# Performance work log

Hardware: AMD Instinct MI355X
Metric: run time of the kernel (lower is better)

## Reference

```python
import jax, jax.numpy as jnp
import numpy as np

DIM = 2048
N_HEADS = 16
HEAD_DIM = DIM // N_HEADS

def setup_inputs() -> dict:
    key = jax.random.key(0)
    kx, kqkv, kout = jax.random.split(key, 3)
    x = jax.random.normal(kx, (2, 2048, DIM), dtype=jnp.float32)
    # nn.Linear weights stored [out_features, in_features]; y = x @ W.T
    W_qkv = jax.random.normal(kqkv, (3 * DIM, DIM), dtype=jnp.float32) * (DIM ** -0.5)
    W_out = jax.random.normal(kout, (DIM, DIM), dtype=jnp.float32) * (DIM ** -0.5)
    return {"x": x, "W_qkv": W_qkv, "W_out": W_out}

def reference(x, W_qkv, W_out):
    B, T, D = x.shape
    qkv = jnp.einsum('btd,ed->bte', x, W_qkv)  # [B,T,3D]
    q, k, v = jnp.split(qkv, 3, axis=-1)
    def heads(t):
        return t.reshape(B, T, N_HEADS, HEAD_DIM).transpose(0, 2, 1, 3)  # [B,H,T,d]
    q, k, v = heads(q), heads(k), heads(v)
    att = jnp.einsum('bhid,bhjd->bhij', q, k) / (HEAD_DIM ** 0.5)
    causal = jnp.tril(jnp.ones((T, T), dtype=bool))
    att = jnp.where(causal, att, -jnp.inf)
    att = jax.nn.softmax(att, axis=-1)
    out = jnp.einsum('bhij,bhjd->bhid', att, v)
    out = out.transpose(0, 2, 1, 3).reshape(B, T, D)
    return jnp.einsum('btd,ed->bte', out, W_out)
```

## Files before the change

kernel.cpp:

```cpp
#include <hip/hip_runtime.h>

typedef short short8 __attribute__((ext_vector_type(8)));
typedef short short4v __attribute__((ext_vector_type(4)));
typedef float f32x4 __attribute__((ext_vector_type(4)));
typedef unsigned short u16;
typedef u16 ushort4v __attribute__((ext_vector_type(4)));

__device__ inline u16 f2bf(float f){
  unsigned int u = __builtin_bit_cast(unsigned int, f);
  u = (u + 0x7fffu + ((u >> 16) & 1u)) >> 16;
  return (u16)u;
}

__device__ inline short8 cat8(short4v a, short4v b){
  short8 r;
  r[0]=a[0]; r[1]=a[1]; r[2]=a[2]; r[3]=a[3];
  r[4]=b[0]; r[5]=b[1]; r[6]=b[2]; r[7]=b[3];
  return r;
}

__device__ inline void gload_lds16(const void* g, unsigned lds_addr){
  __builtin_amdgcn_global_load_lds((__attribute__((address_space(1))) void*)(uintptr_t)g,
                                   (__attribute__((address_space(3))) void*)(uintptr_t)lds_addr,
                                   16, 0, 0);
}

__global__ void cvt_bf16(const float* __restrict__ in, u16* __restrict__ out, int n4){
  int stride = gridDim.x * blockDim.x;
  for (int i = blockIdx.x * blockDim.x + threadIdx.x; i < n4; i += stride){
    float4 v = ((const float4*)in)[i];
    ushort4v r = { f2bf(v.x), f2bf(v.y), f2bf(v.z), f2bf(v.w) };
    ((ushort4v*)out)[i] = r;
  }
}

template<int OUT_BF16>
__global__ __launch_bounds__(512, 2) void gemm_bt2(const u16* __restrict__ A, const u16* __restrict__ B,
                                                   void* __restrict__ Cv, int M, int N, int K){
  __shared__ u16 lds[2][24576];
  const int tid = threadIdx.x, wave = tid >> 6, lane = tid & 63;
  const int lr = lane & 15, lg = lane >> 4;
  const int wm = wave >> 2, wn = wave & 3;
  const long bm = blockIdx.x * 128L, bn = blockIdx.y * 256L;
  const int l3 = lane >> 3, l7 = lane & 7;

  const u16* asrc = A + (bm + wave * 8 + l3) * (long)K + (l7 ^ l3) * 8;
  const u16* bsrc = B + (bn + wave * 8 + l3) * (long)K + (l7 ^ l3) * 8;
  const unsigned ldsbase = (unsigned)(uintptr_t)&lds[0][0];
  const unsigned adst = wave * 1024u;
  const unsigned bdst = 16384u + wave * 1024u;

  #define STAGE(BUF, K0) { \
    unsigned bb = ldsbase + (unsigned)(BUF) * 49152u; \
    gload_lds16(asrc + (K0),                       bb + adst); \
    gload_lds16(asrc + 64 * (size_t)K + (K0),      bb + adst + 8192u); \
    gload_lds16(bsrc + (K0),                       bb + bdst); \
    gload_lds16(bsrc + 64 * (size_t)K + (K0),      bb + bdst + 8192u); \
    gload_lds16(bsrc + 128 * (size_t)K + (K0),     bb + bdst + 16384u); \
    gload_lds16(bsrc + 192 * (size_t)K + (K0),     bb + bdst + 24576u); \
  }

  f32x4 acc[4][4] = {};
  const int nk = K >> 6;
  int cur = 0;

  STAGE(0, 0)
  asm volatile("s_waitcnt vmcnt(0)" ::: "memory");
  __builtin_amdgcn_sched_barrier(0);
  __builtin_amdgcn_s_barrier();
  __builtin_amdgcn_sched_barrier(0);

  for (int t = 0; t < nk; ++t){
    if (t + 1 < nk){
      STAGE(cur ^ 1, (t + 1) * 64)
      asm volatile("s_waitcnt vmcnt(6)" ::: "memory");
    } else {
      asm volatile("s_waitcnt vmcnt(0)" ::: "memory");
    }
    __builtin_amdgcn_sched_barrier(0);
    __builtin_amdgcn_s_barrier();
    __builtin_amdgcn_sched_barrier(0);

    const u16* Ab = &lds[cur][0];
    const u16* Bb = &lds[cur][8192];
    short8 af[2][4], bfr[2][4];
    #pragma unroll
    for (int kk = 0; kk < 2; kk++){
      #pragma unroll
      for (int m = 0; m < 4; m++){
        int row = wm * 64 + m * 16 + lr;
        int phys = (kk * 4 + lg) ^ (row & 7);
        af[kk][m] = *(const short8*)&Ab[row * 64 + phys * 8];
      }
      #pragma unroll
      for (int n = 0; n < 4; n++){
        int row = wn * 64 + n * 16 + lr;
        int phys = (kk * 4 + lg) ^ (row & 7);
        bfr[kk][n] = *(const short8*)&Bb[row * 64 + phys * 8];
      }
    }
    __builtin_amdgcn_s_setprio(1);
    #pragma unroll
    for (int m = 0; m < 4; m++)
      #pragma unroll
      for (int n = 0; n < 4; n++){
        acc[m][n] = __builtin_amdgcn_mfma_f32_16x16x32_bf16(af[0][m], bfr[0][n], acc[m][n], 0, 0, 0);
        acc[m][n] = __builtin_amdgcn_mfma_f32_16x16x32_bf16(af[1][m], bfr[1][n], acc[m][n], 0, 0, 0);
      }
    __builtin_amdgcn_s_setprio(0);

    __builtin_amdgcn_sched_barrier(0);
    __builtin_amdgcn_s_barrier();
    __builtin_amdgcn_sched_barrier(0);
    cur ^= 1;
  }
  #undef STAGE

  #pragma unroll
  for (int m = 0; m < 4; m++){
    #pragma unroll
    for (int n = 0; n < 4; n++){
      #pragma unroll
      for (int r = 0; r < 4; r++){
        long row = bm + wm*64 + m*16 + lg*4 + r;
        long col = bn + wn*64 + n*16 + lr;
        float v = acc[m][n][r];
        if (OUT_BF16) ((u16*)Cv)[row * (long)N + col] = f2bf(v);
        else          ((float*)Cv)[row * (long)N + col] = v;
      }
    }
  }
}

__global__ __launch_bounds__(512, 2) void attn_fwd(const u16* __restrict__ qkv, u16* __restrict__ out){
  const int T = 2048, D3 = 6144, D = 2048, HD = 128;
  const int bh = blockIdx.x;
  const int pr = blockIdx.y;
  const int b = bh >> 4, h = bh & 15;
  const int tid = threadIdx.x, wave = tid >> 6, lane = tid & 63;
  const int lr = lane & 15, lg = lane >> 4;

  __shared__ u16 Klds[64][136];
  __shared__ u16 Vlds[64][136];
  __shared__ u16 Plds[8][16][72];

  const size_t base = (size_t)b * T * D3;
  const unsigned vtr = (unsigned)(uintptr_t)&Vlds[(lane >> 4) * 8 + ((lane >> 2) & 3)][(lane & 3) * 4];

  const int srow = tid >> 4;
  const int scol = (tid & 15) * 8;
  const u16* kgp = qkv + base + (size_t)srow * D3 + D + h * HD + scol;
  const u16* vgp = kgp + D;

  for (int half = 0; half < 2; half++){
    const int qt = half ? pr : (15 - pr);
    const int q0 = qt * 128;
    const int q0w = q0 + wave * 16;

    short8 qf[4];
    {
      const u16* qrow = qkv + base + (size_t)(q0w + lr) * D3 + h * HD;
      #pragma unroll
      for (int kk = 0; kk < 4; kk++)
        qf[kk] = *(const short8*)(qrow + kk*32 + lg*8);
    }

    f32x4 o[8] = {};
    float mrow[4], lrw[4];
    #pragma unroll
    for (int r = 0; r < 4; r++){ mrow[r] = -1e30f; lrw[r] = 0.f; }

    const int ntiles = (q0 + 128) >> 6;
    short8 kreg[2], vreg[2];
    #pragma unroll
    for (int c = 0; c < 2; c++){
      kreg[c] = *(const short8*)(kgp + (size_t)(32 * c) * D3);
      vreg[c] = *(const short8*)(vgp + (size_t)(32 * c) * D3);
    }

    for (int t = 0; t < ntiles; t++){
      const int k0 = t * 64;
      __syncthreads();
      #pragma unroll
      for (int c = 0; c < 2; c++){
        *(short8*)&Klds[srow + 32*c][scol] = kreg[c];
        *(short8*)&Vlds[srow + 32*c][scol] = vreg[c];
      }
      __syncthreads();
      if (t + 1 < ntiles){
        const u16* kn = kgp + (size_t)(k0 + 64) * D3;
        const u16* vn = vgp + (size_t)(k0 + 64) * D3;
        #pragma unroll
        for (int c = 0; c < 2; c++){
          kreg[c] = *(const short8*)(kn + (size_t)(32 * c) * D3);
          vreg[c] = *(const short8*)(vn + (size_t)(32 * c) * D3);
        }
      }

      if (k0 <= q0w + 15){
        f32x4 s[4] = {};
        #pragma unroll
        for (int kh = 0; kh < 4; kh++){
          #pragma unroll
          for (int kk = 0; kk < 4; kk++){
            short8 kfrag = *(const short8*)&Klds[kh*16 + lr][kk*32 + lg*8];
            s[kh] = __builtin_amdgcn_mfma_f32_16x16x32_bf16(qf[kk], kfrag, s[kh], 0, 0, 0);
          }
        }
        const float scale = 0.08838834764831845f;
        const bool need_mask = (k0 + 63 > q0w);
        #pragma unroll
        for (int kh = 0; kh < 4; kh++){
          int key = k0 + kh*16 + lr;
          #pragma unroll
          for (int r = 0; r < 4; r++){
            float v = s[kh][r] * scale;
            if (need_mask && key > q0w + lg*4 + r) v = -1e30f;
            s[kh][r] = v;
          }
        }
        float fs[4];
        #pragma unroll
        for (int r = 0; r < 4; r++){
          float mx = fmaxf(fmaxf(s[0][r], s[1][r]), fmaxf(s[2][r], s[3][r]));
          #pragma unroll
          for (int msk = 8; msk >= 1; msk >>= 1)
            mx = fmaxf(mx, __shfl_xor(mx, msk, 64));
          float mnew = fmaxf(mrow[r], mx);
          float f = __expf(mrow[r] - mnew);
          float p0 = __expf(s[0][r] - mnew);
          float p1 = __expf(s[1][r] - mnew);
          float p2 = __expf(s[2][r] - mnew);
          float p3 = __expf(s[3][r] - mnew);
          s[0][r] = p0; s[1][r] = p1; s[2][r] = p2; s[3][r] = p3;
          float rs = (p0 + p1) + (p2 + p3);
          #pragma unroll
          for (int msk = 8; msk >= 1; msk >>= 1)
            rs += __shfl_xor(rs, msk, 64);
          lrw[r] = lrw[r] * f + rs;
          mrow[r] = mnew;
          fs[r] = f;
        }
        #pragma unroll
        for (int dt = 0; dt < 8; dt++)
          #pragma unroll
          for (int r = 0; r < 4; r++)
            o[dt][r] *= fs[r];
        #pragma unroll
        for (int kh = 0; kh < 4; kh++)
          #pragma unroll
          for (int r = 0; r < 4; r++)
            Plds[wave][lg*4 + r][kh*16 + lr] = f2bf(s[kh][r]);
        asm volatile("s_waitcnt lgkmcnt(0)" ::: "memory");
        __builtin_amdgcn_sched_barrier(0);
        short8 pf[2];
        #pragma unroll
        for (int kp2 = 0; kp2 < 2; kp2++)
          pf[kp2] = *(const short8*)&Plds[wave][lr][kp2*32 + lg*8];
        asm volatile("s_waitcnt lgkmcnt(0)" ::: "memory");
        __builtin_amdgcn_sched_barrier(0);

        short4v vf[2][2][2];
        #define TR4(BUF, PTR) \
          asm volatile("ds_read_b64_tr_b16 %0, %1"             : "=v"(vf[BUF][0][0]) : "v"(PTR)); \
          asm volatile("ds_read_b64_tr_b16 %0, %1 offset:1088" : "=v"(vf[BUF][0][1]) : "v"(PTR)); \
          asm volatile("ds_read_b64_tr_b16 %0, %1 offset:8704" : "=v"(vf[BUF][1][0]) : "v"(PTR)); \
          asm volatile("ds_read_b64_tr_b16 %0, %1 offset:9792" : "=v"(vf[BUF][1][1]) : "v"(PTR));
        TR4(0, vtr)
        #pragma unroll
        for (int dt = 0; dt < 8; dt++){
          if (dt < 7){
            unsigned pn = vtr + (unsigned)((dt + 1) * 32);
            TR4((dt + 1) & 1, pn)
            asm volatile("s_waitcnt lgkmcnt(4)" ::: "memory");
          } else {
            asm volatile("s_waitcnt lgkmcnt(0)" ::: "memory");
          }
          __builtin_amdgcn_sched_barrier(0);
          short8 v0 = cat8(vf[dt & 1][0][0], vf[dt & 1][0][1]);
          short8 v1 = cat8(vf[dt & 1][1][0], vf[dt & 1][1][1]);
          o[dt] = __builtin_amdgcn_mfma_f32_16x16x32_bf16(pf[0], v0, o[dt], 0, 0, 0);
          o[dt] = __builtin_amdgcn_mfma_f32_16x16x32_bf16(pf[1], v1, o[dt], 0, 0, 0);
        }
        #undef TR4
      }
    }
    float rl[4];
    #pragma unroll
    for (int r = 0; r < 4; r++) rl[r] = 1.0f / lrw[r];
    #pragma unroll
    for (int dt = 0; dt < 8; dt++){
      #pragma unroll
      for (int r = 0; r < 4; r++){
        float v = o[dt][r] * rl[r];
        int qa = q0w + lg*4 + r;
        out[(size_t)(b * T + qa) * D + h * HD + dt*16 + lr] = f2bf(v);
      }
    }
  }
}

extern "C" void kernel_launch(void* const* d_in, const int* in_sizes, int n_in,
                              void* d_out, int out_size, void* d_ws, size_t ws_size,
                              hipStream_t stream) {
  const float* x    = (const float*)d_in[0];
  const float* wqkv = (const float*)d_in[1];
  const float* wout = (const float*)d_in[2];
  float* out = (float*)d_out;

  u16* ws    = (u16*)d_ws;
  u16* xb    = ws;
  u16* wqkvb = xb + 8388608;
  u16* qkvb  = wqkvb + 12582912;
  u16* attnb = xb;
  u16* woutb = wqkvb;

  cvt_bf16<<<2048, 256, 0, stream>>>(x,    xb,    8388608 / 4);
  cvt_bf16<<<2048, 256, 0, stream>>>(wqkv, wqkvb, 12582912 / 4);

  gemm_bt2<1><<<dim3(32, 24), 512, 0, stream>>>(xb, wqkvb, qkvb, 4096, 6144, 2048);

  cvt_bf16<<<2048, 256, 0, stream>>>(wout, woutb, 4194304 / 4);

  attn_fwd<<<dim3(32, 8), 512, 0, stream>>>(qkvb, attnb);

  gemm_bt2<0><<<dim3(32, 8), 512, 0, stream>>>(attnb, woutb, out, 4096, 2048, 2048);
}
```

Measured before the change: 268.5 us.

## Use 256x256-tile GEMM with phased split A/B prefetch for QKV projection

```diff
diff --git a/kernel.cpp b/kernel.cpp
--- a/kernel.cpp
+++ b/kernel.cpp
@@ -31,6 +31,92 @@
     float4 v = ((const float4*)in)[i];
     ushort4v r = { f2bf(v.x), f2bf(v.y), f2bf(v.z), f2bf(v.w) };
     ((ushort4v*)out)[i] = r;
+  }
+}
+
+#define BARRIER() { __builtin_amdgcn_sched_barrier(0); __builtin_amdgcn_s_barrier(); __builtin_amdgcn_sched_barrier(0); }
+#define VM4() asm volatile("s_waitcnt vmcnt(4)" ::: "memory");
+
+#define MFMA4(MO, AA, BB) { __builtin_amdgcn_s_setprio(1); \
+  _Pragma("unroll") for (int m = 0; m < 4; m++) \
+    _Pragma("unroll") for (int n = 0; n < 4; n++) \
+      acc[(MO)+m][n] = __builtin_amdgcn_mfma_f32_16x16x32_bf16(AA[(MO)+m], BB[n], acc[(MO)+m][n], 0, 0, 0); \
+  __builtin_amdgcn_s_setprio(0); }
+
+#define PHASE4(ABASE, BBASE, ST1, ST2, ST3, ST4) { \
+    const u16* Ab = (ABASE); const u16* Bb = (BBASE); \
+    short8 a0[8], b0[4], a1[8], b1[4]; \
+    _Pragma("unroll") for (int m = 0; m < 8; m++){ int row = wm*128 + m*16 + lr; int ph = lg ^ (row & 7); a0[m] = *(const short8*)&Ab[row*64 + ph*8]; } \
+    _Pragma("unroll") for (int n = 0; n < 4; n++){ int row = wn*64 + n*16 + lr; int ph = lg ^ (row & 7); b0[n] = *(const short8*)&Bb[row*64 + ph*8]; } \
+    ST1 BARRIER() MFMA4(0, a0, b0) BARRIER() \
+    _Pragma("unroll") for (int m = 0; m < 8; m++){ int row = wm*128 + m*16 + lr; int ph = (4+lg) ^ (row & 7); a1[m] = *(const short8*)&Ab[row*64 + ph*8]; } \
+    _Pragma("unroll") for (int n = 0; n < 4; n++){ int row = wn*64 + n*16 + lr; int ph = (4+lg) ^ (row & 7); b1[n] = *(const short8*)&Bb[row*64 + ph*8]; } \
+    ST2 BARRIER() MFMA4(4, a0, b0) BARRIER() \
+    ST3 BARRIER() MFMA4(0, a1, b1) BARRIER() \
+    ST4 VM4() BARRIER() MFMA4(4, a1, b1) BARRIER() \
+  }
+
+template<int OUT_BF16>
+__global__ __launch_bounds__(512, 2) void gemm256(const u16* __restrict__ A, const u16* __restrict__ B,
+                                                  void* __restrict__ Cv, int M, int N, int K){
+  __shared__ u16 lds[2][32768];
+  const int tid = threadIdx.x, wave = tid >> 6, lane = tid & 63;
+  const int lr = lane & 15, lg = lane >> 4;
+  const int wm = wave >> 2, wn = wave & 3;
+  const long bm = blockIdx.x * 256L, bn = blockIdx.y * 256L;
+  const int l3 = lane >> 3, l7 = lane & 7;
+
+  const u16* asrc = A + (bm + wave*8 + l3) * (long)K + (l7 ^ l3) * 8;
+  const u16* bsrc = B + (bn + wave*8 + l3) * (long)K + (l7 ^ l3) * 8;
+  const unsigned ldsbase = (unsigned)(uintptr_t)&lds[0][0];
+  const unsigned wdst = wave * 1024u;
+
+#define STG_A(BUF,S,KOFF) gload_lds16(asrc + (size_t)(S)*64*K + (KOFF), ldsbase + (BUF)*65536u + wdst + (S)*8192u);
+#define STG_B(BUF,S,KOFF) gload_lds16(bsrc + (size_t)(S)*64*K + (KOFF), ldsbase + (BUF)*65536u + 32768u + wdst + (S)*8192u);
+
+  f32x4 acc[8][4] = {};
+  const int nk = K >> 6;
+
+  #pragma unroll
+  for (int s = 0; s < 4; s++){ STG_A(0, s, 0) }
+  #pragma unroll
+  for (int s = 0; s < 4; s++){ STG_B(0, s, 0) }
+  #pragma unroll
+  for (int s = 0; s < 4; s++){ STG_A(1, s, 64) }
+  VM4()
+  BARRIER()
+
+  for (int i = 0; i < (nk >> 1); i++){
+    const size_t kt1 = (size_t)((2*i + 1) << 6);
+    const size_t kn0 = (size_t)(((2*i + 2) & (nk - 1)) << 6);
+    const size_t kn1 = (size_t)(((2*i + 3) & (nk - 1)) << 6);
+    PHASE4(&lds[0][0], &lds[0][16384],
+           STG_B(1,0,kt1) STG_B(1,1,kt1),
+           STG_B(1,2,kt1) STG_B(1,3,kt1),
+           STG_A(0,0,kn0) STG_A(0,1,kn0),
+           STG_A(0,2,kn0) STG_A(0,3,kn0))
+    PHASE4(&lds[1][0], &lds[1][16384],
+           STG_B(0,0,kn0) STG_B(0,1,kn0),
+           STG_B(0,2,kn0) STG_B(0,3,kn0),
+           STG_A(1,0,kn1) STG_A(1,1,kn1),
+           STG_A(1,2,kn1) STG_A(1,3,kn1))
+  }
+#undef STG_A
+#undef STG_B
+
+  #pragma unroll
+  for (int m = 0; m < 8; m++){
+    #pragma unroll
+    for (int n = 0; n < 4; n++){
+      #pragma unroll
+      for (int r = 0; r < 4; r++){
+        long row = bm + wm*128 + m*16 + lg*4 + r;
+        long col = bn + wn*64 + n*16 + lr;
+        float v = acc[m][n][r];
+        if (OUT_BF16) ((u16*)Cv)[row * (long)N + col] = f2bf(v);
+        else          ((float*)Cv)[row * (long)N + col] = v;
+      }
+    }
   }
 }
 
@@ -66,9 +152,7 @@
 
   STAGE(0, 0)
   asm volatile("s_waitcnt vmcnt(0)" ::: "memory");
-  __builtin_amdgcn_sched_barrier(0);
-  __builtin_amdgcn_s_barrier();
-  __builtin_amdgcn_sched_barrier(0);
+  BARRIER()
 
   for (int t = 0; t < nk; ++t){
     if (t + 1 < nk){
@@ -77,9 +161,7 @@
     } else {
       asm volatile("s_waitcnt vmcnt(0)" ::: "memory");
     }
-    __builtin_amdgcn_sched_barrier(0);
-    __builtin_amdgcn_s_barrier();
-    __builtin_amdgcn_sched_barrier(0);
+    BARRIER()
 
     const u16* Ab = &lds[cur][0];
     const u16* Bb = &lds[cur][8192];
@@ -108,10 +190,7 @@
         acc[m][n] = __builtin_amdgcn_mfma_f32_16x16x32_bf16(af[1][m], bfr[1][n], acc[m][n], 0, 0, 0);
       }
     __builtin_amdgcn_s_setprio(0);
-
-    __builtin_amdgcn_sched_barrier(0);
-    __builtin_amdgcn_s_barrier();
-    __builtin_amdgcn_sched_barrier(0);
+    BARRIER()
     cur ^= 1;
   }
   #undef STAGE
@@ -318,7 +397,7 @@
   cvt_bf16<<<2048, 256, 0, stream>>>(x,    xb,    8388608 / 4);
   cvt_bf16<<<2048, 256, 0, stream>>>(wqkv, wqkvb, 12582912 / 4);
 
-  gemm_bt2<1><<<dim3(32, 24), 512, 0, stream>>>(xb, wqkvb, qkvb, 4096, 6144, 2048);
+  gemm256<1><<<dim3(16, 24), 512, 0, stream>>>(xb, wqkvb, qkvb, 4096, 6144, 2048);
 
   cvt_bf16<<<2048, 256, 0, stream>>>(wout, woutb, 4194304 / 4);
 
```

After: 266.3 us. Within noise of the previous version (-0.8%).
